# Kernel optimization log

Hardware: AMD Instinct MI355X
Metric: run time of the kernel (lower is better)

Reference implementation:

```python
import jax, jax.numpy as jnp
import numpy as np

B, S, H, O, N, R = 16, 1024, 4096, 4096, 8, 64  # batch, seq, in, out, n_adapters, rank
P_DROP = 0.1


def setup_inputs() -> dict:
    key = jax.random.key(0)
    ks = jax.random.split(key, 6)
    result = jax.random.normal(ks[0], (B, S, O), dtype=jnp.float32)  # base-layer output (residual)
    data = jax.random.normal(ks[1], (B, S, H), dtype=jnp.float32)    # hidden states
    keep = 1.0 - P_DROP
    # inverted-dropout mask: values in {0, 1/keep}, reproduces F.dropout(train) exactly
    mask = jax.random.bernoulli(ks[2], keep, (B, S, H)).astype(jnp.float32) / keep
    lora_a = jax.random.normal(ks[3], (N, R, H), dtype=jnp.float32) * 0.02  # per-adapter A
    lora_b = jax.random.normal(ks[4], (N, O, R), dtype=jnp.float32) * 0.02  # per-adapter B
    scalings = jax.random.uniform(ks[5], (N,), dtype=jnp.float32, minval=0.25, maxval=2.0)  # alpha/r per adapter
    return {"result": result, "data": data, "mask": mask,
            "lora_a": lora_a, "lora_b": lora_b, "scalings": scalings}


def reference(result, data, mask, lora_a, lora_b, scalings):
    # Multi-adapter batched LoRA: batch is partitioned into N equal segments,
    # each owned by one adapter. Equivalent to LoraFunction.forward's loop:
    #   drop = dropout(data[s:e]) * scaling; result[s:e] += (drop @ A^T) @ B^T
    per = B // N  # sequences per adapter segment
    x = (data * mask).reshape(N, per, S, H) * scalings[:, None, None, None]
    t = jnp.einsum('npsh,nrh->npsr', x, lora_a)        # [N, per, S, R]
    delta = jnp.einsum('npsr,nor->npso', t, lora_b)    # [N, per, S, O]
    return result + delta.reshape(B, S, O)
```

## Files before the change

### kernel.cpp

```cpp
#include <hip/hip_runtime.h>
#include <hip/hip_bf16.h>


#define B_   16
#define S_   1024
#define H_   4096
#define O_   4096
#define N_   8
#define R_   64
#define ROWS (B_ * S_)
#define ROWS_PER_ADAPTER (ROWS / N_)
#define KSPLIT 2
#define KRANGE (H_ / KSPLIT)

typedef __attribute__((ext_vector_type(8))) short s8v;
typedef __attribute__((ext_vector_type(4))) float f4v;

static __device__ __forceinline__ short f2bf(float f) {
    union { float f; unsigned u; } v; v.f = f;
    unsigned r = (v.u + 0x7FFFu + ((v.u >> 16) & 1u)) >> 16;
    return (short)r;
}

__global__ void cvt_weights(const float* __restrict__ la,
                            const float* __restrict__ lb,
                            const float* __restrict__ scal,
                            short* __restrict__ abf,
                            short* __restrict__ bbf) {
    const int i = blockIdx.x * blockDim.x + threadIdx.x;
    const int A_ELEMS4 = (N_ * R_ * H_) / 4;
    if (i < A_ELEMS4) {
        const int n = i / ((R_ * H_) / 4);
        const float s = scal[n];
        float4 v = ((const float4*)la)[i];
        short4 o;
        o.x = f2bf(v.x * s); o.y = f2bf(v.y * s);
        o.z = f2bf(v.z * s); o.w = f2bf(v.w * s);
        ((short4*)abf)[i] = o;
    } else {
        const int j = i - A_ELEMS4;
        float4 v = ((const float4*)lb)[j];
        short4 o;
        o.x = f2bf(v.x); o.y = f2bf(v.y);
        o.z = f2bf(v.z); o.w = f2bf(v.w);
        ((short4*)bbf)[j] = o;
    }
}

__global__ __launch_bounds__(256, 2)
void lora_k1(const float* __restrict__ data, const float* __restrict__ mask,
             const short* __restrict__ abf, float* __restrict__ tpart) {
    const int tile  = blockIdx.x;
    const int split = blockIdx.y;
    const int w    = threadIdx.x >> 6;
    const int lane = threadIdx.x & 63;
    const int ml   = lane & 15;
    const int g    = lane >> 4;

    const int row0 = tile * 64;
    const int n    = row0 / ROWS_PER_ADAPTER;
    const int row  = row0 + w * 16 + ml;

    const float* dptr = data + (size_t)row * H_ + split * KRANGE + g * 8;
    const float* mptr = mask + (size_t)row * H_ + split * KRANGE + g * 8;
    const short* ap0 = abf + ((size_t)(n * R_ +  0 + ml)) * H_ + split * KRANGE + g * 8;
    const short* ap1 = abf + ((size_t)(n * R_ + 16 + ml)) * H_ + split * KRANGE + g * 8;
    const short* ap2 = abf + ((size_t)(n * R_ + 32 + ml)) * H_ + split * KRANGE + g * 8;
    const short* ap3 = abf + ((size_t)(n * R_ + 48 + ml)) * H_ + split * KRANGE + g * 8;

    f4v acc0 = {0.f, 0.f, 0.f, 0.f};
    f4v acc1 = {0.f, 0.f, 0.f, 0.f};
    f4v acc2 = {0.f, 0.f, 0.f, 0.f};
    f4v acc3 = {0.f, 0.f, 0.f, 0.f};

#pragma unroll 2
    for (int ks = 0; ks < KRANGE / 32; ++ks) {
        float4 d0 = *(const float4*)(dptr);
        float4 d1 = *(const float4*)(dptr + 4);
        float4 m0 = *(const float4*)(mptr);
        float4 m1 = *(const float4*)(mptr + 4);
        s8v a0 = *(const s8v*)(ap0);
        s8v a1 = *(const s8v*)(ap1);
        s8v a2 = *(const s8v*)(ap2);
        s8v a3 = *(const s8v*)(ap3);

        s8v xf;
        xf[0] = f2bf(d0.x * m0.x); xf[1] = f2bf(d0.y * m0.y);
        xf[2] = f2bf(d0.z * m0.z); xf[3] = f2bf(d0.w * m0.w);
        xf[4] = f2bf(d1.x * m1.x); xf[5] = f2bf(d1.y * m1.y);
        xf[6] = f2bf(d1.z * m1.z); xf[7] = f2bf(d1.w * m1.w);

        acc0 = __builtin_amdgcn_mfma_f32_16x16x32_bf16(xf, a0, acc0, 0, 0, 0);
        acc1 = __builtin_amdgcn_mfma_f32_16x16x32_bf16(xf, a1, acc1, 0, 0, 0);
        acc2 = __builtin_amdgcn_mfma_f32_16x16x32_bf16(xf, a2, acc2, 0, 0, 0);
        acc3 = __builtin_amdgcn_mfma_f32_16x16x32_bf16(xf, a3, acc3, 0, 0, 0);

        dptr += 32; mptr += 32;
        ap0 += 32; ap1 += 32; ap2 += 32; ap3 += 32;
    }

    float* tp = tpart + ((size_t)split * ROWS + row0 + w * 16) * R_;
#pragma unroll
    for (int i = 0; i < 4; ++i) {
        tp[(g * 4 + i) * R_ +  0 + ml] = acc0[i];
        tp[(g * 4 + i) * R_ + 16 + ml] = acc1[i];
        tp[(g * 4 + i) * R_ + 32 + ml] = acc2[i];
        tp[(g * 4 + i) * R_ + 48 + ml] = acc3[i];
    }
}

__global__ __launch_bounds__(256, 2)
void lora_k2(const float* __restrict__ result, const float* __restrict__ tpart,
             const short* __restrict__ bbf, float* __restrict__ out) {
    __shared__ short tlds[64 * 80];

    const int tile = blockIdx.x;
    const int oh   = blockIdx.y;
    const int tid  = threadIdx.x;
    const int row0 = tile * 64;
    const int n    = row0 / ROWS_PER_ADAPTER;

    {
        const float* p0 = tpart + (size_t)row0 * R_;
        const float* p1 = tpart + (size_t)ROWS * R_ + (size_t)row0 * R_;
#pragma unroll
        for (int i = 0; i < 4; ++i) {
            const int e  = tid + i * 256;
            const int rw = e >> 4;
            const int r4 = e & 15;
            float4 a = ((const float4*)p0)[e];
            float4 b = ((const float4*)p1)[e];
            short4 o;
            o.x = f2bf(a.x + b.x); o.y = f2bf(a.y + b.y);
            o.z = f2bf(a.z + b.z); o.w = f2bf(a.w + b.w);
            *(short4*)&tlds[rw * 80 + r4 * 4] = o;
        }
    }
    __syncthreads();

    const int w    = tid >> 6;
    const int lane = tid & 63;
    const int ml   = lane & 15;
    const int g    = lane >> 4;

    s8v tf0 = *(const s8v*)&tlds[(w * 16 + ml) * 80 + g * 8];
    s8v tf1 = *(const s8v*)&tlds[(w * 16 + ml) * 80 + g * 8 + 32];

    const short* bptr = bbf + ((size_t)n * O_ + oh * 2048 + ml) * R_ + g * 8;

    const size_t obase0 = (size_t)(row0 + w * 16 + g * 4) * O_ + oh * 2048 + ml;

#pragma unroll 2
    for (int ot = 0; ot < 128; ++ot) {
        s8v bf0 = *(const s8v*)(bptr);
        s8v bf1 = *(const s8v*)(bptr + 32);
        f4v acc = {0.f, 0.f, 0.f, 0.f};
        acc = __builtin_amdgcn_mfma_f32_16x16x32_bf16(tf0, bf0, acc, 0, 0, 0);
        acc = __builtin_amdgcn_mfma_f32_16x16x32_bf16(tf1, bf1, acc, 0, 0, 0);

        const size_t base = obase0 + ot * 16;
#pragma unroll
        for (int i = 0; i < 4; ++i) {
            out[base + (size_t)i * O_] = result[base + (size_t)i * O_] + acc[i];
        }
        bptr += 16 * R_;
    }
}

extern "C" void kernel_launch(void* const* d_in, const int* in_sizes, int n_in,
                              void* d_out, int out_size, void* d_ws, size_t ws_size,
                              hipStream_t stream) {
    const float* result = (const float*)d_in[0];
    const float* data   = (const float*)d_in[1];
    const float* mask   = (const float*)d_in[2];
    const float* lora_a = (const float*)d_in[3];
    const float* lora_b = (const float*)d_in[4];
    const float* scal   = (const float*)d_in[5];
    float* out = (float*)d_out;

    short* abf   = (short*)d_ws;
    short* bbf   = abf + (size_t)N_ * R_ * H_;
    float* tpart = (float*)(bbf + (size_t)N_ * O_ * R_);

    const int cvt_threads = (N_ * R_ * H_ + N_ * O_ * R_) / 4;
    cvt_weights<<<cvt_threads / 256, 256, 0, stream>>>(lora_a, lora_b, scal, abf, bbf);
    lora_k1<<<dim3(ROWS / 64, KSPLIT), 256, 0, stream>>>(data, mask, abf, tpart);
    lora_k2<<<dim3(ROWS / 64, 2), 256, 0, stream>>>(result, tpart, bbf, out);
}
```

Before: 876.6 us.

## Fuse down- and up-projection LoRA kernels into one kernel with LDS reduction

Replaces the two-kernel scheme (down-projection with a global split-K partial buffer, then up-projection) with a single kernel per 16-row tile. Eight waves each compute a 512-wide K slice of the down-projection, reduce the partials through shared memory to a bf16 rank-64 tile, then each wave writes a 512-column output slice. This removes the global round-trip of the intermediate and one launch. The tradeoff is smaller row tiles, so A and B weights are re-read more often per row, and there are extra barriers.

After: 826.2 us. 1.06x faster.

```diff
diff --git a/kernel.cpp b/kernel.cpp
--- a/kernel.cpp
+++ b/kernel.cpp
@@ -1,5 +1,4 @@
 #include <hip/hip_runtime.h>
-#include <hip/hip_bf16.h>
 
 
 #define B_   16
@@ -10,8 +9,6 @@
 #define R_   64
 #define ROWS (B_ * S_)
 #define ROWS_PER_ADAPTER (ROWS / N_)
-#define KSPLIT 2
-#define KRANGE (H_ / KSPLIT)
 
 typedef __attribute__((ext_vector_type(8))) short s8v;
 typedef __attribute__((ext_vector_type(4))) float f4v;
@@ -47,26 +44,30 @@
     }
 }
 
-__global__ __launch_bounds__(256, 2)
-void lora_k1(const float* __restrict__ data, const float* __restrict__ mask,
-             const short* __restrict__ abf, float* __restrict__ tpart) {
-    const int tile  = blockIdx.x;
-    const int split = blockIdx.y;
-    const int w    = threadIdx.x >> 6;
-    const int lane = threadIdx.x & 63;
+__global__ __launch_bounds__(512, 4)
+void lora_fused(const float* __restrict__ data, const float* __restrict__ mask,
+                const short* __restrict__ abf, const short* __restrict__ bbf,
+                const float* __restrict__ result, float* __restrict__ out) {
+    __shared__ float part[8][16][66];
+    __shared__ short tl[16][80];
+
+    const int tile = blockIdx.x;
+    const int row0 = tile * 16;
+    const int n    = row0 / ROWS_PER_ADAPTER;
+    const int tid  = threadIdx.x;
+    const int w    = tid >> 6;
+    const int lane = tid & 63;
     const int ml   = lane & 15;
     const int g    = lane >> 4;
 
-    const int row0 = tile * 64;
-    const int n    = row0 / ROWS_PER_ADAPTER;
-    const int row  = row0 + w * 16 + ml;
-
-    const float* dptr = data + (size_t)row * H_ + split * KRANGE + g * 8;
-    const float* mptr = mask + (size_t)row * H_ + split * KRANGE + g * 8;
-    const short* ap0 = abf + ((size_t)(n * R_ +  0 + ml)) * H_ + split * KRANGE + g * 8;
-    const short* ap1 = abf + ((size_t)(n * R_ + 16 + ml)) * H_ + split * KRANGE + g * 8;
-    const short* ap2 = abf + ((size_t)(n * R_ + 32 + ml)) * H_ + split * KRANGE + g * 8;
-    const short* ap3 = abf + ((size_t)(n * R_ + 48 + ml)) * H_ + split * KRANGE + g * 8;
+    const int row = row0 + ml;
+    const int k0  = w * 512 + g * 8;
+    const float* dptr = data + (size_t)row * H_ + k0;
+    const float* mptr = mask + (size_t)row * H_ + k0;
+    const short* ap0 = abf + (size_t)(n * R_ +  0 + ml) * H_ + k0;
+    const short* ap1 = abf + (size_t)(n * R_ + 16 + ml) * H_ + k0;
+    const short* ap2 = abf + (size_t)(n * R_ + 32 + ml) * H_ + k0;
+    const short* ap3 = abf + (size_t)(n * R_ + 48 + ml) * H_ + k0;
 
     f4v acc0 = {0.f, 0.f, 0.f, 0.f};
     f4v acc1 = {0.f, 0.f, 0.f, 0.f};
@@ -74,7 +75,7 @@
     f4v acc3 = {0.f, 0.f, 0.f, 0.f};
 
 #pragma unroll 2
-    for (int ks = 0; ks < KRANGE / 32; ++ks) {
+    for (int ks = 0; ks < 512 / 32; ++ks) {
         float4 d0 = *(const float4*)(dptr);
         float4 d1 = *(const float4*)(dptr + 4);
         float4 m0 = *(const float4*)(mptr);
@@ -99,66 +100,45 @@
         ap0 += 32; ap1 += 32; ap2 += 32; ap3 += 32;
     }
 
-    float* tp = tpart + ((size_t)split * ROWS + row0 + w * 16) * R_;
 #pragma unroll
     for (int i = 0; i < 4; ++i) {
-        tp[(g * 4 + i) * R_ +  0 + ml] = acc0[i];
-        tp[(g * 4 + i) * R_ + 16 + ml] = acc1[i];
-        tp[(g * 4 + i) * R_ + 32 + ml] = acc2[i];
-        tp[(g * 4 + i) * R_ + 48 + ml] = acc3[i];
-    }
-}
-
-__global__ __launch_bounds__(256, 2)
-void lora_k2(const float* __restrict__ result, const float* __restrict__ tpart,
-             const short* __restrict__ bbf, float* __restrict__ out) {
-    __shared__ short tlds[64 * 80];
-
-    const int tile = blockIdx.x;
-    const int oh   = blockIdx.y;
-    const int tid  = threadIdx.x;
-    const int row0 = tile * 64;
-    const int n    = row0 / ROWS_PER_ADAPTER;
-
-    {
-        const float* p0 = tpart + (size_t)row0 * R_;
-        const float* p1 = tpart + (size_t)ROWS * R_ + (size_t)row0 * R_;
-#pragma unroll
-        for (int i = 0; i < 4; ++i) {
-            const int e  = tid + i * 256;
-            const int rw = e >> 4;
-            const int r4 = e & 15;
-            float4 a = ((const float4*)p0)[e];
-            float4 b = ((const float4*)p1)[e];
-            short4 o;
-            o.x = f2bf(a.x + b.x); o.y = f2bf(a.y + b.y);
-            o.z = f2bf(a.z + b.z); o.w = f2bf(a.w + b.w);
-            *(short4*)&tlds[rw * 80 + r4 * 4] = o;
-        }
+        part[w][g * 4 + i][ 0 + ml] = acc0[i];
+        part[w][g * 4 + i][16 + ml] = acc1[i];
+        part[w][g * 4 + i][32 + ml] = acc2[i];
+        part[w][g * 4 + i][48 + ml] = acc3[i];
     }
     __syncthreads();
 
-    const int w    = tid >> 6;
-    const int lane = tid & 63;
-    const int ml   = lane & 15;
-    const int g    = lane >> 4;
+    {
+        const int e0 = tid * 2;
+        const int rw = e0 >> 6;
+        const int c  = e0 & 63;
+        float s0 = 0.f, s1 = 0.f;
+#pragma unroll
+        for (int p = 0; p < 8; ++p) {
+            float2 v = *(const float2*)&part[p][rw][c];
+            s0 += v.x; s1 += v.y;
+        }
+        tl[rw][c]     = f2bf(s0);
+        tl[rw][c + 1] = f2bf(s1);
+    }
+    __syncthreads();
 
-    s8v tf0 = *(const s8v*)&tlds[(w * 16 + ml) * 80 + g * 8];
-    s8v tf1 = *(const s8v*)&tlds[(w * 16 + ml) * 80 + g * 8 + 32];
+    s8v tf0 = *(const s8v*)&tl[ml][g * 8];
+    s8v tf1 = *(const s8v*)&tl[ml][g * 8 + 32];
 
-    const short* bptr = bbf + ((size_t)n * O_ + oh * 2048 + ml) * R_ + g * 8;
-
-    const size_t obase0 = (size_t)(row0 + w * 16 + g * 4) * O_ + oh * 2048 + ml;
+    const short* bptr = bbf + ((size_t)n * O_ + w * 512 + ml) * R_ + g * 8;
+    const size_t obase0 = (size_t)(row0 + g * 4) * O_ + w * 512 + ml;
 
 #pragma unroll 2
-    for (int ot = 0; ot < 128; ++ot) {
+    for (int ot = 0; ot < 32; ++ot) {
         s8v bf0 = *(const s8v*)(bptr);
         s8v bf1 = *(const s8v*)(bptr + 32);
         f4v acc = {0.f, 0.f, 0.f, 0.f};
         acc = __builtin_amdgcn_mfma_f32_16x16x32_bf16(tf0, bf0, acc, 0, 0, 0);
         acc = __builtin_amdgcn_mfma_f32_16x16x32_bf16(tf1, bf1, acc, 0, 0, 0);
 
-        const size_t base = obase0 + ot * 16;
+        const size_t base = obase0 + (size_t)ot * 16;
 #pragma unroll
         for (int i = 0; i < 4; ++i) {
             out[base + (size_t)i * O_] = result[base + (size_t)i * O_] + acc[i];
@@ -178,12 +158,10 @@
     const float* scal   = (const float*)d_in[5];
     float* out = (float*)d_out;
 
-    short* abf   = (short*)d_ws;
-    short* bbf   = abf + (size_t)N_ * R_ * H_;
-    float* tpart = (float*)(bbf + (size_t)N_ * O_ * R_);
+    short* abf = (short*)d_ws;
+    short* bbf = abf + (size_t)N_ * R_ * H_;
 
     const int cvt_threads = (N_ * R_ * H_ + N_ * O_ * R_) / 4;
     cvt_weights<<<cvt_threads / 256, 256, 0, stream>>>(lora_a, lora_b, scal, abf, bbf);
-    lora_k1<<<dim3(ROWS / 64, KSPLIT), 256, 0, stream>>>(data, mask, abf, tpart);
-    lora_k2<<<dim3(ROWS / 64, 2), 256, 0, stream>>>(result, tpart, bbf, out);
+    lora_fused<<<dim3(ROWS / 16), 512, 0, stream>>>(data, mask, abf, bbf, result, out);
 }
```
